# Kernel optimization log

Measured on AMD Instinct MI355X. Metric: run time of the kernel, lower is better.

## Reference

```python
import jax, jax.numpy as jnp
import numpy as np

N_ATOMS = 10000
N_PAIRS = 160000
F = 256   # number_of_per_atom_features
G = 16    # number_of_radial_basis_functions
H = 64    # number_of_vector_features
HID = 256
MLP_IN = F + H + F + H  # 640 (is_first_module=False)
MLP_OUT = F + 2         # 258


def _gelu(x):
    return jax.nn.gelu(x, approximate=False)


def setup_inputs() -> dict:
    key = jax.random.key(0)
    ks = jax.random.split(key, 16)
    inp = {
        "atomic_embedding": jax.random.normal(ks[0], (N_ATOMS, F), dtype=jnp.float32),
        "partial_charges": jax.random.normal(ks[1], (N_ATOMS, 1), dtype=jnp.float32),
        "pair_indices": jax.random.randint(ks[2], (2, N_PAIRS), 0, N_ATOMS),
        "gs": jax.random.normal(ks[3], (N_PAIRS, G), dtype=jnp.float32),
        "gv": jax.random.normal(ks[4], (N_PAIRS, 3, G), dtype=jnp.float32),
        "agh": jax.random.normal(ks[5], (F, G, H), dtype=jnp.float32) * 0.1,
        # gs_to_fatom: Linear(G -> F, bias=False); torch weight layout [out, in]
        "W_gs": jax.random.normal(ks[6], (F, G), dtype=jnp.float32) * (1.0 / np.sqrt(G)),
        # MLP: 640 -> 256 (gelu) -> 256 (gelu) -> 258 (linear)
        "W1": jax.random.normal(ks[7], (HID, MLP_IN), dtype=jnp.float32) * (1.0 / np.sqrt(MLP_IN)),
        "b1": jnp.zeros((HID,), dtype=jnp.float32),
        "W2": jax.random.normal(ks[8], (HID, HID), dtype=jnp.float32) * (1.0 / np.sqrt(HID)),
        "b2": jnp.zeros((HID,), dtype=jnp.float32),
        "W3": jax.random.normal(ks[9], (MLP_OUT, HID), dtype=jnp.float32) * (1.0 / np.sqrt(HID)),
        "b3": jnp.zeros((MLP_OUT,), dtype=jnp.float32),
    }
    return inp


def reference(atomic_embedding, partial_charges, pair_indices, gs, gv, agh,
              W_gs, W1, b1, W2, b2, W3, b3):
    n_atoms = atomic_embedding.shape[0]
    idx_j = pair_indices[1]

    # gather per-pair atomic features
    a_j = atomic_embedding[idx_j]                      # [P, F]
    q_j = partial_charges[idx_j]                       # [P, 1]

    # radial contributions (embedding branch)
    mapped_gs = gs @ W_gs.T                            # [P, F]
    radial_emb = jax.ops.segment_sum(a_j * mapped_gs, idx_j, num_segments=n_atoms)  # [N, F]

    # vector contributions: einsum('pa,pdg,agh->phd') done pairwise
    m = jnp.einsum('pa,agh->pgh', a_j, agh)            # [P, G, H]
    avf_v = jnp.einsum('pgh,pdg->phd', m, gv)          # [P, H, 3]
    avf_v_sum = jax.ops.segment_sum(avf_v, idx_j, num_segments=n_atoms)  # [N, H, 3]
    vector_emb = jnp.linalg.norm(avf_v_sum, axis=-1)   # [N, H]

    # charge branch: radial only, vector contributions are zeros
    radial_q = jax.ops.segment_sum(q_j * mapped_gs, idx_j, num_segments=n_atoms)    # [N, F]
    vector_q = jnp.zeros((n_atoms, H), dtype=atomic_embedding.dtype)

    combined = jnp.concatenate([radial_emb, vector_emb, radial_q, vector_q], axis=1)  # [N, 640]

    h = _gelu(combined @ W1.T + b1)
    h = _gelu(h @ W2.T + b2)
    out = h @ W3.T + b3                                # [N, F+2]

    delta_q = out[:, 0:1]
    f = out[:, 1:2]
    delta_a = out[:, 2:]
    return (delta_a, delta_q, f)
```

## Files before the change

### kernel.cpp

```cpp
#include <hip/hip_runtime.h>
#include <hip/hip_bf16.h>
#include <math.h>

#define N_ATOMS 10000
#define N_PAIRS 160000
#define FDIM 256
#define GDIM 16
#define HDIM 64
#define HIDDIM 256
#define MLP_IN 640
#define MLP_OUT 258

typedef __attribute__((ext_vector_type(8))) short short8;
typedef __attribute__((ext_vector_type(4))) unsigned short u16x4;
typedef __attribute__((ext_vector_type(4))) float f32x4;

#define MFMA16(a, b, c) __builtin_amdgcn_mfma_f32_16x16x32_bf16((a), (b), (c), 0, 0, 0)


__device__ __forceinline__ float gelu_exact(float x) {
    return 0.5f * x * (1.0f + erff(x * 0.70710678118654752f));
}
__device__ __forceinline__ short bf16bits(float x) {
    __hip_bfloat16 h = __float2bfloat16(x);
    return *reinterpret_cast<short*>(&h);
}
__device__ __forceinline__ float bf2f(unsigned short u) {
    return __uint_as_float(((unsigned)u) << 16);
}
__device__ __forceinline__ short8 cvt8(f32x4 v0, f32x4 v1) {
    short8 o;
    o[0] = bf16bits(v0[0]); o[1] = bf16bits(v0[1]);
    o[2] = bf16bits(v0[2]); o[3] = bf16bits(v0[3]);
    o[4] = bf16bits(v1[0]); o[5] = bf16bits(v1[1]);
    o[6] = bf16bits(v1[2]); o[7] = bf16bits(v1[3]);
    return o;
}

#define PV_W1  18432
#define PV_W2  8192
#define PV_AGH 32768
#define PV_W3  10240
#define PV_CNT 10000
#define PREP_TOTAL (PV_W1 + PV_W2 + PV_AGH + PV_W3 + PV_CNT)
__global__ void prep_kernel(const float* __restrict__ W1,
                            const float* __restrict__ W2,
                            const float* __restrict__ agh,
                            const float* __restrict__ W3,
                            short* __restrict__ W1t,
                            short* __restrict__ W2t,
                            short* __restrict__ aghTt,
                            short* __restrict__ W3t,
                            int* __restrict__ cnt) {
    int tid = blockIdx.x * blockDim.x + threadIdx.x;
    if (tid >= PREP_TOTAL) return;
    int j = tid;
    if (j < PV_W1) {
        int n = j / 72, k8 = j % 72;
        int dst = (((n >> 4) * 18 + (k8 >> 2)) * 4 + (k8 & 3)) * 128 + (n & 15) * 8;
        const float* src = W1 + n * 640 + k8 * 8;
        *(short8*)(W1t + dst) = cvt8(*(const f32x4*)src, *(const f32x4*)(src + 4));
        return;
    }
    j -= PV_W1;
    if (j < PV_W2) {
        int n = j >> 5, k8 = j & 31;
        int dst = (((n >> 4) * 8 + (k8 >> 2)) * 4 + (k8 & 3)) * 128 + (n & 15) * 8;
        const float* src = W2 + n * 256 + k8 * 8;
        *(short8*)(W2t + dst) = cvt8(*(const f32x4*)src, *(const f32x4*)(src + 4));
        return;
    }
    j -= PV_W2;
    if (j < PV_AGH) {
        int n = j >> 5, k8 = j & 31;
        int k0 = k8 * 8;
        short8 o;
#pragma unroll
        for (int i = 0; i < 8; ++i)
            o[i] = bf16bits(agh[(long long)(k0 + i) * 1024 + n]);
        int dst = (((n >> 4) * 8 + (k8 >> 2)) * 4 + (k8 & 3)) * 128 + (n & 15) * 8;
        *(short8*)(aghTt + dst) = o;
        return;
    }
    j -= PV_AGH;
    if (j < PV_W3) {
        int n = j >> 5, k8 = j & 31;
        int dst = (((n >> 4) * 8 + (k8 >> 2)) * 4 + (k8 & 3)) * 128 + (n & 15) * 8;
        if (n < MLP_OUT) {
            const float* src = W3 + n * 256 + k8 * 8;
            *(short8*)(W3t + dst) = cvt8(*(const f32x4*)src, *(const f32x4*)(src + 4));
        } else {
            short8 z = {};
            *(short8*)(W3t + dst) = z;
        }
        return;
    }
    j -= PV_W3;
    cnt[j] = 0;
}

__global__ void hist_kernel(const int* __restrict__ idx_j, int* __restrict__ cnt) {
    int p = blockIdx.x * blockDim.x + threadIdx.x;
    if (p >= N_PAIRS) return;
    atomicAdd(&cnt[idx_j[p]], 1);
}

__global__ __launch_bounds__(1024) void scan_kernel(const int* __restrict__ cnt,
                                                    int* __restrict__ start,
                                                    int* __restrict__ cursor) {
    __shared__ int part[1024];
    int t = threadIdx.x;
    int base = t * 10;
    int pre[10];
    int sum = 0;
#pragma unroll
    for (int k = 0; k < 10; ++k) {
        int i = base + k;
        int v = (i < N_ATOMS) ? cnt[i] : 0;
        pre[k] = sum;
        sum += v;
    }
    part[t] = sum;
    __syncthreads();
    for (int off = 1; off < 1024; off <<= 1) {
        int v = (t >= off) ? part[t - off] : 0;
        __syncthreads();
        part[t] += v;
        __syncthreads();
    }
    int excl = (t == 0) ? 0 : part[t - 1];
#pragma unroll
    for (int k = 0; k < 10; ++k) {
        int i = base + k;
        if (i < N_ATOMS) {
            start[i]  = excl + pre[k];
            cursor[i] = excl + pre[k];
        }
    }
}

__global__ void scatter_data_kernel(const int* __restrict__ idx_j,
                                    int* __restrict__ cursor,
                                    const float* __restrict__ gs,
                                    const float* __restrict__ gv,
                                    __hip_bfloat16* __restrict__ prS) {
    int p = blockIdx.x * blockDim.x + threadIdx.x;
    if (p >= N_PAIRS) return;
    int i = idx_j[p];
    int pos = atomicAdd(&cursor[i], 1);
    short* dst = (short*)prS + (long long)pos * 64;
    const float* g1 = gs + (long long)p * 16;
    *(short8*)(dst)     = cvt8(*(const f32x4*)(g1),     *(const f32x4*)(g1 + 4));
    *(short8*)(dst + 8) = cvt8(*(const f32x4*)(g1 + 8), *(const f32x4*)(g1 + 12));
    const float* g2 = gv + (long long)p * 48;
#pragma unroll
    for (int k = 0; k < 6; ++k)
        *(short8*)(dst + 16 + k * 8) =
            cvt8(*(const f32x4*)(g2 + k * 8), *(const f32x4*)(g2 + k * 8 + 4));
}

__global__ __launch_bounds__(256) void gatherM_build(
        const __hip_bfloat16* __restrict__ prS,
        const int* __restrict__ start,
        const int* __restrict__ cnt,
        const float* __restrict__ emb,
        const float* __restrict__ q,
        const float* __restrict__ W_gs,
        const short* __restrict__ aghTt,
        short* __restrict__ comb_t) {
    __shared__ float sW[FDIM * 17];
    __shared__ short sE[16][264];
    __shared__ float sG[16][GDIM];
    __shared__ float sGV[16][48];
    int i0 = blockIdx.x * 16;
    int mb = blockIdx.x;
    int t = threadIdx.x;

    for (int j = t; j < FDIM * GDIM; j += 256)
        sW[(j >> 4) * 17 + (j & 15)] = W_gs[j];

    {
        int r = t >> 4, cb = (t & 15) * 16;
        const float* src = emb + (long long)(i0 + r) * FDIM + cb;
        *(short8*)(&sE[r][cb])     = cvt8(*(const f32x4*)(src),     *(const f32x4*)(src + 4));
        *(short8*)(&sE[r][cb + 8]) = cvt8(*(const f32x4*)(src + 8), *(const f32x4*)(src + 12));
    }

    {
        int grp = t >> 4, l = t & 15;
        int atom = i0 + grp;
        int s = start[atom], c = cnt[atom];
        const unsigned short* base = (const unsigned short*)prS + (long long)s * 64 + l * 4;
        f32x4 acc = {0.f, 0.f, 0.f, 0.f};
        int j = 0;
        for (; j + 1 < c; j += 2) {
            u16x4 v0 = *(const u16x4*)(base + (long long)j * 64);
            u16x4 v1 = *(const u16x4*)(base + (long long)(j + 1) * 64);
            acc[0] += bf2f(v0[0]) + bf2f(v1[0]);
            acc[1] += bf2f(v0[1]) + bf2f(v1[1]);
            acc[2] += bf2f(v0[2]) + bf2f(v1[2]);
            acc[3] += bf2f(v0[3]) + bf2f(v1[3]);
        }
        if (j < c) {
            u16x4 v0 = *(const u16x4*)(base + (long long)j * 64);
            acc[0] += bf2f(v0[0]);
            acc[1] += bf2f(v0[1]);
            acc[2] += bf2f(v0[2]);
            acc[3] += bf2f(v0[3]);
        }
        if (l < 4) *(f32x4*)&sG[grp][l * 4] = acc;
        else       *(f32x4*)&sGV[grp][(l - 4) * 4] = acc;
    }
    __syncthreads();

    {
        float wreg[GDIM];
#pragma unroll
        for (int g = 0; g < GDIM; ++g) wreg[g] = sW[t * 17 + g];
        int kb1 = t >> 5, kg1 = (t >> 3) & 3, ke1 = t & 7;
        int k2 = 320 + t;
        int kb2 = k2 >> 5, kg2 = (k2 >> 3) & 3, ke2 = k2 & 7;
        long long b1f = (((long long)mb * 18 + kb1) * 4 + kg1) * 128 + ke1;
        long long b2f = (((long long)mb * 18 + kb2) * 4 + kg2) * 128 + ke2;
#pragma unroll 4
        for (int a = 0; a < 16; ++a) {
            int i = i0 + a;
            float S = 0.f;
#pragma unroll
            for (int g = 0; g < GDIM; ++g) S += sG[a][g] * wreg[g];
            float ev = emb[(long long)i * FDIM + t];
            float qq = q[i];
            comb_t[b1f + a * 8] = bf16bits(ev * S);
            comb_t[b2f + a * 8] = bf16bits(qq * S);
        }
    }

    {
        int lane = t & 63, wave = t >> 6;
        int lr = lane & 15;
        int ko = (lane >> 4) * 8;
        int rbase = (lane >> 4) * 4;

        short8 af[8];
#pragma unroll
        for (int ks = 0; ks < 8; ++ks)
            af[ks] = *(const short8*)(&sE[lr][ks * 32 + ko]);

        float U0[4] = {}, U1[4] = {}, U2[4] = {};
#pragma unroll
        for (int g = 0; g < 16; ++g) {
            f32x4 acc = {0.f, 0.f, 0.f, 0.f};
            int nb = g * 4 + wave;
            const short* Bb = aghTt + (long long)nb * 8 * 512 + lane * 8;
#pragma unroll
            for (int kb = 0; kb < 8; ++kb) {
                short8 b = *(const short8*)(Bb + kb * 512);
                acc = MFMA16(af[kb], b, acc);
            }
#pragma unroll
            for (int r = 0; r < 4; ++r) {
                int a = rbase + r;
                U0[r] += acc[r] * sGV[a][g];
                U1[r] += acc[r] * sGV[a][16 + g];
                U2[r] += acc[r] * sGV[a][32 + g];
            }
        }
        int off = wave * 16 + lr;
        int kb = 8 + (off >> 5), kg = (off >> 3) & 3, ke = off & 7;
        long long bf = (((long long)mb * 18 + kb) * 4 + kg) * 128 + ke;
#pragma unroll
        for (int r = 0; r < 4; ++r) {
            int a = rbase + r;
            float v = sqrtf(U0[r] * U0[r] + U1[r] * U1[r] + U2[r] * U2[r]);
            comb_t[bf + a * 8] = bf16bits(v);
        }
    }
}

__global__ __launch_bounds__(512) void mlp_fused(
        const short* __restrict__ comb_t,
        const short* __restrict__ W1t,
        const short* __restrict__ W2t,
        const short* __restrict__ W3t,
        const float* __restrict__ b1,
        const float* __restrict__ b2,
        const float* __restrict__ b3,
        float* __restrict__ outp) {
    __shared__ short h1s[32][264];
    __shared__ short h2s[32][264];
    int lane = threadIdx.x & 63;
    int wave = threadIdx.x >> 6;
    int m0 = blockIdx.x * 32;
    int mbb = blockIdx.x * 2;
    int lr = lane & 15;
    int ko = (lane >> 4) * 8;
    int rbase = (lane >> 4) * 4;

    const short* At[2];
#pragma unroll
    for (int fm = 0; fm < 2; ++fm) {
        int mb = mbb + fm;
        if (mb > 624) mb = 624;
        At[fm] = comb_t + (long long)mb * 18 * 512 + lane * 8;
    }

    {
        f32x4 acc[2][2] = {};
        const short* Bt = W1t + (long long)(wave * 2) * 18 * 512 + lane * 8;
#pragma unroll 3
        for (int kbi = 0; kbi < 18; ++kbi) {
            short8 a[2], b[2];
#pragma unroll
            for (int fm = 0; fm < 2; ++fm) a[fm] = *(const short8*)(At[fm] + kbi * 512);
#pragma unroll
            for (int fn = 0; fn < 2; ++fn)
                b[fn] = *(const short8*)(Bt + fn * 18 * 512 + kbi * 512);
#pragma unroll
            for (int fm = 0; fm < 2; ++fm)
#pragma unroll
                for (int fn = 0; fn < 2; ++fn)
                    acc[fm][fn] = MFMA16(a[fm], b[fn], acc[fm][fn]);
        }
#pragma unroll
        for (int fn = 0; fn < 2; ++fn) {
            int col = wave * 32 + fn * 16 + lr;
            float bias = b1[col];
#pragma unroll
            for (int fm = 0; fm < 2; ++fm)
#pragma unroll
                for (int r = 0; r < 4; ++r)
                    h1s[fm * 16 + rbase + r][col] = bf16bits(gelu_exact(acc[fm][fn][r] + bias));
        }
    }
    __syncthreads();

    {
        f32x4 acc[2][2] = {};
        const short* Bt = W2t + (long long)(wave * 2) * 8 * 512 + lane * 8;
#pragma unroll
        for (int kbi = 0; kbi < 8; ++kbi) {
            short8 a[2], b[2];
#pragma unroll
            for (int fm = 0; fm < 2; ++fm)
                a[fm] = *(const short8*)(&h1s[fm * 16 + lr][ko + kbi * 32]);
#pragma unroll
            for (int fn = 0; fn < 2; ++fn)
                b[fn] = *(const short8*)(Bt + fn * 8 * 512 + kbi * 512);
#pragma unroll
            for (int fm = 0; fm < 2; ++fm)
#pragma unroll
                for (int fn = 0; fn < 2; ++fn)
                    acc[fm][fn] = MFMA16(a[fm], b[fn], acc[fm][fn]);
        }
#pragma unroll
        for (int fn = 0; fn < 2; ++fn) {
            int col = wave * 32 + fn * 16 + lr;
            float bias = b2[col];
#pragma unroll
            for (int fm = 0; fm < 2; ++fm)
#pragma unroll
                for (int r = 0; r < 4; ++r)
                    h2s[fm * 16 + rbase + r][col] = bf16bits(gelu_exact(acc[fm][fn][r] + bias));
        }
    }
    __syncthreads();

    {
        int f0 = wave, f1 = wave + 8, f2 = wave + 16;
        bool has2 = (wave < 4);
        f32x4 acc0[2] = {}, acc1[2] = {}, acc2[2] = {};
        const short* B0 = W3t + (long long)f0 * 8 * 512 + lane * 8;
        const short* B1 = W3t + (long long)f1 * 8 * 512 + lane * 8;
        const short* B2 = W3t + (long long)(has2 ? f2 : f0) * 8 * 512 + lane * 8;
#pragma unroll
        for (int kbi = 0; kbi < 8; ++kbi) {
            short8 a[2];
#pragma unroll
            for (int fm = 0; fm < 2; ++fm)
                a[fm] = *(const short8*)(&h2s[fm * 16 + lr][ko + kbi * 32]);
            short8 b0 = *(const short8*)(B0 + kbi * 512);
            short8 b1v = *(const short8*)(B1 + kbi * 512);
#pragma unroll
            for (int fm = 0; fm < 2; ++fm) {
                acc0[fm] = MFMA16(a[fm], b0, acc0[fm]);
                acc1[fm] = MFMA16(a[fm], b1v, acc1[fm]);
            }
            if (has2) {
                short8 b2v = *(const short8*)(B2 + kbi * 512);
#pragma unroll
                for (int fm = 0; fm < 2; ++fm)
                    acc2[fm] = MFMA16(a[fm], b2v, acc2[fm]);
            }
        }
#pragma unroll
        for (int slot = 0; slot < 3; ++slot) {
            if (slot == 2 && !has2) continue;
            int f = (slot == 0) ? f0 : (slot == 1) ? f1 : f2;
            int col = f * 16 + lr;
            if (col >= MLP_OUT) continue;
            float bias = b3[col];
#pragma unroll
            for (int fm = 0; fm < 2; ++fm) {
#pragma unroll
                for (int r = 0; r < 4; ++r) {
                    int row = m0 + fm * 16 + rbase + r;
                    if (row >= N_ATOMS) continue;
                    f32x4 av = (slot == 0) ? acc0[fm] : (slot == 1) ? acc1[fm] : acc2[fm];
                    float v = av[r] + bias;
                    if (col == 0)      outp[2560000 + row] = v;
                    else if (col == 1) outp[2570000 + row] = v;
                    else               outp[(long long)row * 256 + (col - 2)] = v;
                }
            }
        }
    }
}

extern "C" void kernel_launch(void* const* d_in, const int* in_sizes, int n_in,
                              void* d_out, int out_size, void* d_ws, size_t ws_size,
                              hipStream_t stream) {
    const float* emb  = (const float*)d_in[0];
    const float* q    = (const float*)d_in[1];
    const int*   pidx = (const int*)d_in[2];
    const float* gs   = (const float*)d_in[3];
    const float* gv   = (const float*)d_in[4];
    const float* agh  = (const float*)d_in[5];
    const float* W_gs = (const float*)d_in[6];
    const float* W1   = (const float*)d_in[7];
    const float* b1   = (const float*)d_in[8];
    const float* W2   = (const float*)d_in[9];
    const float* b2   = (const float*)d_in[10];
    const float* W3   = (const float*)d_in[11];
    const float* b3   = (const float*)d_in[12];
    float* out = (float*)d_out;
    float* ws  = (float*)d_ws;

    int*   cnt    = (int*)(ws);
    int*   startA = (int*)(ws + 10000);
    int*   cursor = (int*)(ws + 20000);
    __hip_bfloat16* prS = (__hip_bfloat16*)(ws + 30000);
    short* aghTt = (short*)(ws + 5150000);
    short* W1t   = (short*)(ws + 5281072);
    short* W2t   = (short*)(ws + 5354800);
    short* W3t   = (short*)(ws + 5387568);
    short* comb_t= (short*)(ws + 5428528);

    const int* idx_j = pidx + N_PAIRS;

    {
        int blocks = (PREP_TOTAL + 255) / 256;
        prep_kernel<<<blocks, 256, 0, stream>>>(W1, W2, agh, W3,
                                                W1t, W2t, aghTt, W3t, cnt);
    }
    {
        int blocks = (N_PAIRS + 255) / 256;
        hist_kernel<<<blocks, 256, 0, stream>>>(idx_j, cnt);
        scan_kernel<<<1, 1024, 0, stream>>>(cnt, startA, cursor);
        scatter_data_kernel<<<blocks, 256, 0, stream>>>(idx_j, cursor, gs, gv, prS);
    }
    gatherM_build<<<625, 256, 0, stream>>>(
        prS, startA, cnt, emb, q, W_gs, aghTt, comb_t);
    mlp_fused<<<(N_ATOMS + 31) / 32, 512, 0, stream>>>(
        comb_t, W1t, W2t, W3t, b1, b2, b3, out);
}
```

Before: 104.5 us.

## Fold charge radial branch into W1 via precomputed W1·W_gs and drop zero columns

Because radial_q equals q times (G @ W_gs^T) and vector_q is all zeros, the charge branch's contribution to the first MLP layer reduces to q·G multiplied by W1[:,320:576]·W_gs. The prep kernel now precomputes that 256x16 product and packs it into a single extra K block, and the zero vector_q columns are dropped. This shrinks the layer-1 K dimension from 18 to 11 blocks and removes the per-atom 256-wide charge writes from the build kernel. The exchange is an extra small reduction in prep and a different rounding order for the charge path in bf16.

```diff
diff --git a/kernel.cpp b/kernel.cpp
--- a/kernel.cpp
+++ b/kernel.cpp
@@ -10,6 +10,7 @@
 #define HIDDIM 256
 #define MLP_IN 640
 #define MLP_OUT 258
+#define KB1 11
 
 typedef __attribute__((ext_vector_type(8))) short short8;
 typedef __attribute__((ext_vector_type(4))) unsigned short u16x4;
@@ -37,13 +38,16 @@
     return o;
 }
 
-#define PV_W1  18432
+#define PV_W1M 10240
+#define PV_V1  4096
+#define PV_W1Z 512
 #define PV_W2  8192
 #define PV_AGH 32768
 #define PV_W3  10240
 #define PV_CNT 10000
-#define PREP_TOTAL (PV_W1 + PV_W2 + PV_AGH + PV_W3 + PV_CNT)
+#define PREP_TOTAL (PV_W1M + PV_V1 + PV_W1Z + PV_W2 + PV_AGH + PV_W3 + PV_CNT)
 __global__ void prep_kernel(const float* __restrict__ W1,
+                            const float* __restrict__ W_gs,
                             const float* __restrict__ W2,
                             const float* __restrict__ agh,
                             const float* __restrict__ W3,
@@ -55,14 +59,34 @@
     int tid = blockIdx.x * blockDim.x + threadIdx.x;
     if (tid >= PREP_TOTAL) return;
     int j = tid;
-    if (j < PV_W1) {
-        int n = j / 72, k8 = j % 72;
-        int dst = (((n >> 4) * 18 + (k8 >> 2)) * 4 + (k8 & 3)) * 128 + (n & 15) * 8;
+    if (j < PV_W1M) {
+        int n = j / 40, k8 = j % 40;
+        int dst = (((n >> 4) * KB1 + (k8 >> 2)) * 4 + (k8 & 3)) * 128 + (n & 15) * 8;
         const float* src = W1 + n * 640 + k8 * 8;
         *(short8*)(W1t + dst) = cvt8(*(const f32x4*)src, *(const f32x4*)(src + 4));
         return;
     }
-    j -= PV_W1;
+    j -= PV_W1M;
+    if (j < PV_V1) {
+        int n = j >> 4, g = j & 15;
+        const float* wrow = W1 + n * 640 + 320;
+        float acc = 0.f;
+#pragma unroll 8
+        for (int f = 0; f < 256; ++f)
+            acc += wrow[f] * W_gs[f * 16 + g];
+        int dst = (((n >> 4) * KB1 + 10) * 4 + (g >> 3)) * 128 + (n & 15) * 8 + (g & 7);
+        W1t[dst] = bf16bits(acc);
+        return;
+    }
+    j -= PV_V1;
+    if (j < PV_W1Z) {
+        int n = j >> 1, oct = j & 1;
+        int dst = (((n >> 4) * KB1 + 10) * 4 + (2 + oct)) * 128 + (n & 15) * 8;
+        short8 z = {};
+        *(short8*)(W1t + dst) = z;
+        return;
+    }
+    j -= PV_W1Z;
     if (j < PV_W2) {
         int n = j >> 5, k8 = j & 31;
         int dst = (((n >> 4) * 8 + (k8 >> 2)) * 4 + (k8 & 3)) * 128 + (n & 15) * 8;
@@ -218,10 +242,7 @@
 #pragma unroll
         for (int g = 0; g < GDIM; ++g) wreg[g] = sW[t * 17 + g];
         int kb1 = t >> 5, kg1 = (t >> 3) & 3, ke1 = t & 7;
-        int k2 = 320 + t;
-        int kb2 = k2 >> 5, kg2 = (k2 >> 3) & 3, ke2 = k2 & 7;
-        long long b1f = (((long long)mb * 18 + kb1) * 4 + kg1) * 128 + ke1;
-        long long b2f = (((long long)mb * 18 + kb2) * 4 + kg2) * 128 + ke2;
+        long long b1f = (((long long)mb * KB1 + kb1) * 4 + kg1) * 128 + ke1;
 #pragma unroll 4
         for (int a = 0; a < 16; ++a) {
             int i = i0 + a;
@@ -229,10 +250,14 @@
 #pragma unroll
             for (int g = 0; g < GDIM; ++g) S += sG[a][g] * wreg[g];
             float ev = emb[(long long)i * FDIM + t];
-            float qq = q[i];
             comb_t[b1f + a * 8] = bf16bits(ev * S);
-            comb_t[b2f + a * 8] = bf16bits(qq * S);
-        }
+        }
+        int a = t >> 4, g = t & 15;
+        float val = q[i0 + a] * sG[a][g];
+        long long oq = (((long long)mb * KB1 + 10) * 4 + (g >> 3)) * 128 + a * 8 + (g & 7);
+        long long oz = (((long long)mb * KB1 + 10) * 4 + 2 + (g >> 3)) * 128 + a * 8 + (g & 7);
+        comb_t[oq] = bf16bits(val);
+        comb_t[oz] = bf16bits(0.f);
     }
 
     {
@@ -267,7 +292,7 @@
         }
         int off = wave * 16 + lr;
         int kb = 8 + (off >> 5), kg = (off >> 3) & 3, ke = off & 7;
-        long long bf = (((long long)mb * 18 + kb) * 4 + kg) * 128 + ke;
+        long long bf = (((long long)mb * KB1 + kb) * 4 + kg) * 128 + ke;
 #pragma unroll
         for (int r = 0; r < 4; ++r) {
             int a = rbase + r;
@@ -301,20 +326,20 @@
     for (int fm = 0; fm < 2; ++fm) {
         int mb = mbb + fm;
         if (mb > 624) mb = 624;
-        At[fm] = comb_t + (long long)mb * 18 * 512 + lane * 8;
+        At[fm] = comb_t + (long long)mb * KB1 * 512 + lane * 8;
     }
 
     {
         f32x4 acc[2][2] = {};
-        const short* Bt = W1t + (long long)(wave * 2) * 18 * 512 + lane * 8;
+        const short* Bt = W1t + (long long)(wave * 2) * KB1 * 512 + lane * 8;
 #pragma unroll 3
-        for (int kbi = 0; kbi < 18; ++kbi) {
+        for (int kbi = 0; kbi < KB1; ++kbi) {
             short8 a[2], b[2];
 #pragma unroll
             for (int fm = 0; fm < 2; ++fm) a[fm] = *(const short8*)(At[fm] + kbi * 512);
 #pragma unroll
             for (int fn = 0; fn < 2; ++fn)
-                b[fn] = *(const short8*)(Bt + fn * 18 * 512 + kbi * 512);
+                b[fn] = *(const short8*)(Bt + fn * KB1 * 512 + kbi * 512);
 #pragma unroll
             for (int fm = 0; fm < 2; ++fm)
 #pragma unroll
@@ -441,15 +466,15 @@
     __hip_bfloat16* prS = (__hip_bfloat16*)(ws + 30000);
     short* aghTt = (short*)(ws + 5150000);
     short* W1t   = (short*)(ws + 5281072);
-    short* W2t   = (short*)(ws + 5354800);
-    short* W3t   = (short*)(ws + 5387568);
-    short* comb_t= (short*)(ws + 5428528);
+    short* W2t   = (short*)(ws + 5326128);
+    short* W3t   = (short*)(ws + 5358896);
+    short* comb_t= (short*)(ws + 5399856);
 
     const int* idx_j = pidx + N_PAIRS;
 
     {
         int blocks = (PREP_TOTAL + 255) / 256;
-        prep_kernel<<<blocks, 256, 0, stream>>>(W1, W2, agh, W3,
+        prep_kernel<<<blocks, 256, 0, stream>>>(W1, W_gs, W2, agh, W3,
                                                 W1t, W2t, aghTt, W3t, cnt);
     }
     {
```

New measurement: 128.6 us. +23.1%, slower.
